# Performance work log

Hardware: AMD Instinct MI355X
Metric: run time of the kernel (lower is better)

## Reference

```python
import jax, jax.numpy as jnp
import numpy as np
from math import factorial, sqrt

L_MAX = 3
MUL = 64
# e3nn FullyConnectedTensorProduct instruction order: lexicographic over (l1, l2, l3)
# keeping paths with triangle inequality and matching parity ((-1)^(l1+l2) == (-1)^l3).
PATHS = [(l1, l2, l3)
         for l1 in range(L_MAX + 1)
         for l2 in range(L_MAX + 1)
         for l3 in range(L_MAX + 1)
         if abs(l1 - l2) <= l3 <= l1 + l2 and (l1 + l2 + l3) % 2 == 0]
assert len(PATHS) == 23
N_TO = {l3: sum(1 for p in PATHS if p[2] == l3) for l3 in range(L_MAX + 1)}


def _su2_cg(j1, m1, j2, m2, j3, m3):
    # Complex-basis Clebsch-Gordan coefficient (Racah formula), as in e3nn.
    if m3 != m1 + m2:
        return 0.0
    f = factorial
    vmin = max(-j1 + j2 + m3, -j1 + m1, 0)
    vmax = min(j2 + j3 + m1, j3 - j1 + j2, j3 + m3)
    c = sqrt((2 * j3 + 1) * f(j3 + j1 - j2) * f(j3 - j1 + j2) * f(j1 + j2 - j3)
             * f(j3 + m3) * f(j3 - m3)
             / (f(j1 + j2 + j3 + 1) * f(j1 - m1) * f(j1 + m1) * f(j2 - m2) * f(j2 + m2)))
    s = 0.0
    for v in range(vmin, vmax + 1):
        s += (-1) ** (v + j2 + m2) / f(v) * f(j2 + j3 + m1 - v) * f(j1 - m1 + v) \
             / f(j3 - j1 + j2 - v) / f(j3 + m3 - v) / f(v + j1 - j2 - m3)
    return c * s


def _q(l):
    # Change of basis real -> complex spherical harmonics (e3nn convention).
    q = np.zeros((2 * l + 1, 2 * l + 1), dtype=np.complex128)
    for m in range(-l, 0):
        q[l + m, l + abs(m)] = 1.0 / np.sqrt(2.0)
        q[l + m, l - abs(m)] = -1j / np.sqrt(2.0)
    q[l, l] = 1.0
    for m in range(1, l + 1):
        q[l + m, l + abs(m)] = (-1) ** m / np.sqrt(2.0)
        q[l + m, l - abs(m)] = 1j * (-1) ** m / np.sqrt(2.0)
    return (-1j) ** l * q


def _w3j(l1, l2, l3):
    # Real-basis Wigner 3j tensor, unit Frobenius norm (e3nn's o3.wigner_3j).
    csu2 = np.zeros((2 * l1 + 1, 2 * l2 + 1, 2 * l3 + 1))
    for m1 in range(-l1, l1 + 1):
        for m2 in range(-l2, l2 + 1):
            m3 = m1 + m2
            if -l3 <= m3 <= l3:
                csu2[l1 + m1, l2 + m2, l3 + m3] = _su2_cg(l1, m1, l2, m2, l3, m3)
    q1, q2, q3 = _q(l1), _q(l2), _q(l3)
    c = np.einsum('ij,kl,mn,ikn->jlm', q1, q2, np.conj(q3.T), csu2.astype(np.complex128))
    c = np.real(c)
    return (c / np.linalg.norm(c)).astype(np.float32)


W3J = {p: jnp.asarray(_w3j(*p)) for p in PATHS}
# e3nn 'component' irrep_normalization + 'element' path_normalization:
# per-path coeff = sqrt(ir_out.dim / (n_paths_into_out * mul1 * mul2)).
COEFF = {p: float(np.sqrt((2 * p[2] + 1) / (N_TO[p[2]] * MUL * MUL))) for p in PATHS}


def setup_inputs():
    key = jax.random.key(0)
    kx, kw = jax.random.split(key)
    x = jax.random.normal(kx, (2, 1024, MUL * (L_MAX + 1) ** 2), dtype=jnp.float32)
    weights = jax.random.normal(kw, (len(PATHS), MUL, MUL, MUL), dtype=jnp.float32)
    return {"x": x, "weights": weights}


def reference(x, weights):
    B, N, D = x.shape
    Z = B * N
    xf = x.reshape(Z, D)
    # e3nn layout: blocks of (mul, 2l+1) concatenated over l; offset = MUL * l^2.
    xs = [xf[:, MUL * l * l: MUL * (l + 1) ** 2].reshape(Z, MUL, 2 * l + 1)
          for l in range(L_MAX + 1)]
    acc = [jnp.zeros((Z, MUL, 2 * l + 1), dtype=x.dtype) for l in range(L_MAX + 1)]
    for p, (l1, l2, l3) in enumerate(PATHS):
        c = W3J[(l1, l2, l3)]
        t1 = jnp.einsum('zui,ijk->zujk', xs[l1], c)            # [Z,u,2l2+1,2l3+1]
        t2 = jnp.einsum('zujk,zvj->zuvk', t1, xs[l2])          # [Z,u,v,2l3+1]
        seg = jnp.einsum('zuvk,uvw->zwk', t2, weights[p]) * COEFF[(l1, l2, l3)]
        acc[l3] = acc[l3] + seg
    out = jnp.concatenate([a.reshape(Z, -1) for a in acc], axis=-1)
    return out.reshape(B, N, -1)
```

## Files before the change

kernel.cpp:

```cpp
#include <hip/hip_runtime.h>

struct CD { double re, im; };
constexpr CD cmul(CD a, CD b){ return CD{a.re*b.re - a.im*b.im, a.re*b.im + a.im*b.re}; }
constexpr CD conj_(CD a){ return CD{a.re, -a.im}; }

constexpr double factd(int n){ double r = 1.0; for(int i = 2; i <= n; ++i) r *= (double)i; return r; }
constexpr double csqrt_(double x){
  if (x <= 0.0) return 0.0;
  double g = x > 1.0 ? x : 1.0;
  for (int i = 0; i < 100; ++i) g = 0.5*(g + x/g);
  return g;
}

constexpr double su2_cg(int j1,int m1,int j2,int m2,int j3,int m3){
  if (m3 != m1 + m2) return 0.0;
  int vmin = -j1 + j2 + m3;
  if (-j1 + m1 > vmin) vmin = -j1 + m1;
  if (0 > vmin) vmin = 0;
  int vmax = j2 + j3 + m1;
  if (j3 - j1 + j2 < vmax) vmax = j3 - j1 + j2;
  if (j3 + m3 < vmax) vmax = j3 + m3;
  double c = csqrt_((2.0*j3 + 1.0) * factd(j3 + j1 - j2) * factd(j3 - j1 + j2) * factd(j1 + j2 - j3)
                    * factd(j3 + m3) * factd(j3 - m3)
                    / (factd(j1 + j2 + j3 + 1) * factd(j1 - m1) * factd(j1 + m1)
                       * factd(j2 - m2) * factd(j2 + m2)));
  double s = 0.0;
  for (int v = vmin; v <= vmax; ++v){
    double t = (((v + j2 + m2) & 1) ? -1.0 : 1.0) / factd(v)
               * factd(j2 + j3 + m1 - v) * factd(j1 - m1 + v)
               / factd(j3 - j1 + j2 - v) / factd(j3 + m3 - v) / factd(v + j1 - j2 - m3);
    s += t;
  }
  return c * s;
}

struct QM { CD m[7][7]; };
constexpr QM qmat(int l){
  QM q{};
  double is2 = 1.0 / csqrt_(2.0);
  for (int mm = -l; mm < 0; ++mm){
    q.m[l+mm][l-mm] = CD{is2, 0.0};
    q.m[l+mm][l+mm] = CD{0.0, -is2};
  }
  q.m[l][l] = CD{1.0, 0.0};
  for (int mm = 1; mm <= l; ++mm){
    double sgn = (mm & 1) ? -1.0 : 1.0;
    q.m[l+mm][l+mm] = CD{sgn*is2, 0.0};
    q.m[l+mm][l-mm] = CD{0.0, sgn*is2};
  }
  CD ph = (l % 4 == 0) ? CD{1,0} : (l % 4 == 1) ? CD{0,-1} : (l % 4 == 2) ? CD{-1,0} : CD{0,1};
  for (int r = 0; r < 7; ++r)
    for (int c = 0; c < 7; ++c)
      q.m[r][c] = cmul(ph, q.m[r][c]);
  return q;
}

template<int L1,int L2,int L3> struct W3JT { float v[2*L1+1][2*L2+1][2*L3+1]; };

template<int L1,int L2,int L3>
constexpr W3JT<L1,L2,L3> make_w3j(){
  constexpr int D1 = 2*L1+1, D2 = 2*L2+1, D3 = 2*L3+1;
  QM q1 = qmat(L1), q2 = qmat(L2), q3 = qmat(L3);
  double cg[7][7] = {};
  for (int i = 0; i < D1; ++i)
    for (int k = 0; k < D2; ++k){
      int n = i + k - L1 - L2 + L3;
      if (n >= 0 && n < D3) cg[i][k] = su2_cg(L1, i-L1, L2, k-L2, L3, (i-L1)+(k-L2));
    }
  double c[D1][D2][D3] = {};
  double norm2 = 0.0;
  for (int j = 0; j < D1; ++j)
    for (int l = 0; l < D2; ++l)
      for (int m = 0; m < D3; ++m){
        CD s{0.0, 0.0};
        for (int i = 0; i < D1; ++i)
          for (int k = 0; k < D2; ++k){
            double g = cg[i][k];
            if (g == 0.0) continue;
            int n = i + k - L1 - L2 + L3;
            CD t = cmul(q1.m[i][j], q2.m[k][l]);
            t = cmul(t, conj_(q3.m[n][m]));
            s.re += t.re * g; s.im += t.im * g;
          }
        c[j][l][m] = s.re;
        norm2 += s.re * s.re;
      }
  double inv = 1.0 / csqrt_(norm2);
  W3JT<L1,L2,L3> w{};
  for (int j = 0; j < D1; ++j)
    for (int l = 0; l < D2; ++l)
      for (int m = 0; m < D3; ++m){
        double val = c[j][l][m] * inv;
        if (val < 1e-10 && val > -1e-10) val = 0.0;
        w.v[j][l][m] = (float)val;
      }
  return w;
}

__device__ __constant__ int L3P_[23]  = {0,1,2,3,1,0,2,1,3,2,2,1,3,0,2,1,3,3,2,1,3,0,2};
__device__ __constant__ int SWAPP_[23] = {0,1,1,1,0,0,0,1,1,1,0,0,0,0,0,1,1,0,0,0,0,0,0};
constexpr int K3CUM[24] = {0,1,4,9,16,19,20,25,28,35,40,45,48,55,56,61,64,71,78,83,86,93,94,99};
constexpr size_t KSLICE = 2048ull * 64ull;

typedef __bf16 bf16x8 __attribute__((ext_vector_type(8)));
typedef float  f32x4  __attribute__((ext_vector_type(4)));
typedef float  f32x2  __attribute__((ext_vector_type(2)));

__global__ void pack_w_kernel(const float* __restrict__ w, unsigned short* __restrict__ wp, int total){
  int idx = blockIdx.x * 256 + threadIdx.x;
  if (idx >= total) return;
  int e    = idx & 7;
  int lane = (idx >> 3) & 63;
  int nt   = (idx >> 9) & 3;
  int hf   = (idx >> 11) & 1;
  int s    = (idx >> 12) & 63;
  int p    = idx >> 18;
  int kv = hf*32 + (lane >> 4)*8 + e;
  int wc = nt*16 + (lane & 15);
  int l3 = L3P_[p];
  const float nto[4] = {4.f, 6.f, 7.f, 6.f};
  float coeff = sqrtf((2.f*l3 + 1.f) / (nto[l3] * 4096.f));
  int a = SWAPP_[p] ? kv : s;
  int b = SWAPP_[p] ? s : kv;
  float val = w[(((size_t)p*64 + a)*64 + b)*64 + wc] * coeff;
  unsigned bits = __builtin_bit_cast(unsigned, val);
  unsigned r = (bits + 0x7FFFu + ((bits >> 16) & 1u)) >> 16;
  wp[idx] = (unsigned short)r;
}

__global__ void transpose_x(const float* __restrict__ x, float* __restrict__ xT){
  __shared__ float t[32][33];
  int bx = blockIdx.x, by = blockIdx.y;
  int tx = threadIdx.x & 31, ty = threadIdx.x >> 5;
  #pragma unroll
  for (int r = 0; r < 4; ++r)
    t[ty + r*8][tx] = x[(size_t)(by*32 + ty + r*8)*1024 + bx*32 + tx];
  __syncthreads();
  #pragma unroll
  for (int r = 0; r < 4; ++r)
    xT[(size_t)(bx*32 + ty + r*8)*2048 + by*32 + tx] = t[tx][ty + r*8];
}

template<int P,int L1,int L2,int L3,bool SWAP,int G0,int G,bool PART>
__device__ __forceinline__ void run_slot(
    int tile, const float* __restrict__ xT,
    const unsigned short* __restrict__ wp,
    float* __restrict__ dst, float* red)
{
  constexpr int K3 = 2*L3+1;
  constexpr int LK = SWAP ? L1 : L2;
  constexpr int LS = SWAP ? L2 : L1;
  constexpr int DK = 2*LK+1, DS = 2*LS+1;
  constexpr auto C = make_w3j<L1,L2,L3>();

  const int lane = threadIdx.x & 63;
  const int wv   = threadIdx.x >> 6;
  const int zc   = tile*16 + (lane & 15);

  f32x2 xk2[4][DK];
  {
    const float* xkb = xT + (size_t)(64*LK*LK)*2048 + zc;
    const int t0 = wv*32 + (lane >> 4)*8;
    #pragma unroll
    for (int q = 0; q < 4; ++q)
      #pragma unroll
      for (int t = 0; t < DK; ++t){
        float lo = xkb[(size_t)((t0 + 2*q    )*DK + t)*2048];
        float hi = xkb[(size_t)((t0 + 2*q + 1)*DK + t)*2048];
        xk2[q][t] = f32x2{lo, hi};
      }
  }

  const float* xsb = xT + (size_t)(64*LS*LS)*2048 + zc;
  const unsigned short* wu = wp + (size_t)P*262144 + (size_t)wv*2048 + (size_t)lane*8;

  f32x4 acc[G][4];
  #pragma unroll
  for (int a = 0; a < G; ++a)
    #pragma unroll
    for (int b = 0; b < 4; ++b) acc[a][b] = f32x4{0.f,0.f,0.f,0.f};

  auto compute = [&](const bf16x8 (&bf)[4], const float (&xs)[DS]){
    #pragma unroll
    for (int kk = 0; kk < G; ++kk){
      float dk[DK];
      #pragma unroll
      for (int t = 0; t < DK; ++t) dk[t] = 0.f;
      #pragma unroll
      for (int t = 0; t < DK; ++t){
        #pragma unroll
        for (int j = 0; j < DS; ++j){
          const float cv = SWAP ? C.v[t][j][G0+kk] : C.v[j][t][G0+kk];
          if (cv != 0.0f) dk[t] = __builtin_fmaf(xs[j], cv, dk[t]);
        }
      }
      f32x2 af2[4];
      #pragma unroll
      for (int q = 0; q < 4; ++q) af2[q] = f32x2{0.f, 0.f};
      #pragma unroll
      for (int t = 0; t < DK; ++t){
        const f32x2 d2 = f32x2{dk[t], dk[t]};
        #pragma unroll
        for (int q = 0; q < 4; ++q)
          af2[q] += xk2[q][t] * d2;
      }
      bf16x8 af;
      #pragma unroll
      for (int q = 0; q < 4; ++q){
        af[2*q]   = (__bf16)af2[q].x;
        af[2*q+1] = (__bf16)af2[q].y;
      }
      __builtin_amdgcn_s_setprio(1);
      #pragma unroll
      for (int nt = 0; nt < 4; ++nt)
        acc[kk][nt] = __builtin_amdgcn_mfma_f32_16x16x32_bf16(af, bf[nt], acc[kk][nt], 0, 0, 0);
      __builtin_amdgcn_s_setprio(0);
    }
  };

  bf16x8 bA[4], bB[4];
  float xsA[DS], xsB[DS];
  #pragma unroll
  for (int nt = 0; nt < 4; ++nt)
    bA[nt] = *reinterpret_cast<const bf16x8*>(wu + nt*512);
  #pragma unroll
  for (int j = 0; j < DS; ++j) xsA[j] = xsb[(size_t)j*2048];

  for (int s = 0; s < 64; s += 2){
    #pragma unroll
    for (int nt = 0; nt < 4; ++nt)
      bB[nt] = *reinterpret_cast<const bf16x8*>(wu + 4096 + nt*512);
    #pragma unroll
    for (int j = 0; j < DS; ++j) xsB[j] = xsb[(size_t)(DS + j)*2048];

    compute(bA, xsA);

    #pragma unroll
    for (int nt = 0; nt < 4; ++nt)
      bA[nt] = *reinterpret_cast<const bf16x8*>(wu + 8192 + nt*512);
    #pragma unroll
    for (int j = 0; j < DS; ++j) xsA[j] = xsb[(size_t)(2*DS + j)*2048];

    compute(bB, xsB);

    wu  += 8192;
    xsb += (size_t)2*DS*2048;
  }

  constexpr int Gh = (G + 1) / 2;
  static_assert(Gh <= 3, "red[] sized for Gh<=3");
  auto store_one = [&](int kk, int nt, const f32x4& o, const f32x4& a){
    #pragma unroll
    for (int r = 0; r < 4; ++r){
      int zl = ((lane >> 4) << 2) + r;
      int wc = nt*16 + (lane & 15);
      float val = a[r] + o[r];
      if constexpr (PART){
        dst[(size_t)(K3CUM[P] + G0 + kk)*KSLICE + (size_t)(tile*16 + zl)*64 + wc] = val;
      } else {
        unsafeAtomicAdd(dst + (size_t)(tile*16 + zl)*1024 + 64*L3*L3 + wc*K3 + (G0+kk), val);
      }
    }
  };

  if (wv == 1){
    #pragma unroll
    for (int kk = 0; kk < Gh; ++kk)
      #pragma unroll
      for (int nt = 0; nt < 4; ++nt)
        *reinterpret_cast<f32x4*>(&red[((kk*4 + nt)*64 + lane)*4]) = acc[kk][nt];
  }
  __syncthreads();
  if (wv == 0){
    #pragma unroll
    for (int kk = 0; kk < Gh; ++kk)
      #pragma unroll
      for (int nt = 0; nt < 4; ++nt){
        f32x4 o = *reinterpret_cast<const f32x4*>(&red[((kk*4 + nt)*64 + lane)*4]);
        store_one(kk, nt, o, acc[kk][nt]);
      }
  }
  if constexpr (G > Gh){
    if (wv == 0){
      #pragma unroll
      for (int kk = Gh; kk < G; ++kk)
        #pragma unroll
        for (int nt = 0; nt < 4; ++nt)
          *reinterpret_cast<f32x4*>(&red[(((kk-Gh)*4 + nt)*64 + lane)*4]) = acc[kk][nt];
    }
    __syncthreads();
    if (wv == 1){
      #pragma unroll
      for (int kk = Gh; kk < G; ++kk)
        #pragma unroll
        for (int nt = 0; nt < 4; ++nt){
          f32x4 o = *reinterpret_cast<const f32x4*>(&red[(((kk-Gh)*4 + nt)*64 + lane)*4]);
          store_one(kk, nt, o, acc[kk][nt]);
        }
    }
  }
}

template<bool PART>
__global__ __launch_bounds__(128, 3) void tp_main(const float* __restrict__ xT,
    const unsigned short* __restrict__ wp, float* __restrict__ dst)
{
  __shared__ __align__(16) float red[3072];
  const int slot = blockIdx.x >> 7;
  const int tile = blockIdx.x & 127;
  switch (slot){
    case 0:  run_slot< 6,1,1,2,false,0,5,PART>(tile,xT,wp,dst,red); break;
    case 1:  run_slot<16,2,3,3,true ,0,3,PART>(tile,xT,wp,dst,red); break;
    case 2:  run_slot<20,3,2,3,false,0,3,PART>(tile,xT,wp,dst,red); break;
    case 3:  run_slot<14,2,2,2,false,0,3,PART>(tile,xT,wp,dst,red); break;
    case 4:  run_slot<15,2,3,1,true ,0,3,PART>(tile,xT,wp,dst,red); break;
    case 5:  run_slot<19,3,2,1,false,0,3,PART>(tile,xT,wp,dst,red); break;
    case 6:  run_slot< 8,1,2,3,true ,0,4,PART>(tile,xT,wp,dst,red); break;
    case 7:  run_slot<12,2,1,3,false,0,4,PART>(tile,xT,wp,dst,red); break;
    case 8:  run_slot<22,3,3,2,false,0,2,PART>(tile,xT,wp,dst,red); break;
    case 9:  run_slot<22,3,3,2,false,2,2,PART>(tile,xT,wp,dst,red); break;
    case 10: run_slot< 9,1,3,2,true ,0,3,PART>(tile,xT,wp,dst,red); break;
    case 11: run_slot<16,2,3,3,true ,3,2,PART>(tile,xT,wp,dst,red); break;
    case 12: run_slot<16,2,3,3,true ,5,2,PART>(tile,xT,wp,dst,red); break;
    case 13: run_slot<20,3,2,3,false,3,2,PART>(tile,xT,wp,dst,red); break;
    case 14: run_slot<20,3,2,3,false,5,2,PART>(tile,xT,wp,dst,red); break;
    case 15: run_slot< 2,0,2,2,true ,0,5,PART>(tile,xT,wp,dst,red); break;
    case 16: run_slot<10,2,0,2,false,0,5,PART>(tile,xT,wp,dst,red); break;
    case 17: run_slot<11,2,1,1,false,0,3,PART>(tile,xT,wp,dst,red); break;
    case 18: run_slot< 7,1,2,1,true ,0,3,PART>(tile,xT,wp,dst,red); break;
    case 19: run_slot<18,3,1,2,false,0,3,PART>(tile,xT,wp,dst,red); break;
    case 20: run_slot< 8,1,2,3,true ,4,3,PART>(tile,xT,wp,dst,red); break;
    case 21: run_slot<12,2,1,3,false,4,3,PART>(tile,xT,wp,dst,red); break;
    case 22: run_slot<14,2,2,2,false,3,2,PART>(tile,xT,wp,dst,red); break;
    case 23: run_slot< 9,1,3,2,true ,3,2,PART>(tile,xT,wp,dst,red); break;
    case 24: run_slot<18,3,1,2,false,3,2,PART>(tile,xT,wp,dst,red); break;
    case 25: run_slot<22,3,3,2,false,4,1,PART>(tile,xT,wp,dst,red); break;
    case 26: run_slot<21,3,3,0,false,0,1,PART>(tile,xT,wp,dst,red); break;
    case 27: run_slot< 3,0,3,3,true ,0,4,PART>(tile,xT,wp,dst,red); break;
    case 28: run_slot<17,3,0,3,false,0,4,PART>(tile,xT,wp,dst,red); break;
    case 29: run_slot< 3,0,3,3,true ,4,3,PART>(tile,xT,wp,dst,red); break;
    case 30: run_slot<17,3,0,3,false,4,3,PART>(tile,xT,wp,dst,red); break;
    case 31: run_slot< 1,0,1,1,true ,0,3,PART>(tile,xT,wp,dst,red); break;
    case 32: run_slot< 4,1,0,1,false,0,3,PART>(tile,xT,wp,dst,red); break;
    case 33: run_slot<13,2,2,0,false,0,1,PART>(tile,xT,wp,dst,red); break;
    case 34: run_slot< 5,1,1,0,false,0,1,PART>(tile,xT,wp,dst,red); break;
    case 35: run_slot< 0,0,0,0,false,0,1,PART>(tile,xT,wp,dst,red); break;
    default: break;
  }
}

__global__ void gather_out(const float* __restrict__ part, float* __restrict__ out){
  const int z = blockIdx.x;
  const int t = threadIdx.x;
  const int w = t & 63;
  const int g = t >> 6;
  const size_t zw = (size_t)z*64 + w;
  const float* pb = part;
  auto rd = [&](int kg){ return pb[(size_t)kg*KSLICE + zw]; };
  float* ob = out + (size_t)z*1024;
  if (g == 0){
    ob[w] = rd(K3CUM[0]) + rd(K3CUM[5]) + rd(K3CUM[13]) + rd(K3CUM[21]);
  } else if (g == 1){
    #pragma unroll
    for (int k = 0; k < 3; ++k)
      ob[64 + w*3 + k] = rd(K3CUM[1]+k) + rd(K3CUM[4]+k) + rd(K3CUM[7]+k)
                       + rd(K3CUM[11]+k) + rd(K3CUM[15]+k) + rd(K3CUM[19]+k);
  } else if (g == 2){
    #pragma unroll
    for (int k = 0; k < 5; ++k)
      ob[256 + w*5 + k] = rd(K3CUM[2]+k) + rd(K3CUM[6]+k) + rd(K3CUM[9]+k)
                        + rd(K3CUM[10]+k) + rd(K3CUM[14]+k) + rd(K3CUM[18]+k)
                        + rd(K3CUM[22]+k);
  } else {
    #pragma unroll
    for (int k = 0; k < 7; ++k)
      ob[576 + w*7 + k] = rd(K3CUM[3]+k) + rd(K3CUM[8]+k) + rd(K3CUM[12]+k)
                        + rd(K3CUM[16]+k) + rd(K3CUM[17]+k) + rd(K3CUM[20]+k);
  }
}

extern "C" void kernel_launch(void* const* d_in, const int* in_sizes, int n_in,
                              void* d_out, int out_size, void* d_ws, size_t ws_size,
                              hipStream_t stream)
{
  const float* x = (const float*)d_in[0];
  const float* w = (const float*)d_in[1];
  float* out = (float*)d_out;

  const size_t packB = 23ull*64*2*4*64*8 * sizeof(unsigned short);
  const size_t xTB   = 1024ull*2048*sizeof(float);
  const size_t partB = 99ull*KSLICE*sizeof(float);
  const size_t slack = 65536;
  const int totalW = 23*64*2*4*64*8;

  unsigned short* wp = (unsigned short*)d_ws;
  float* xT   = (float*)((char*)d_ws + packB);
  float* part = (float*)((char*)d_ws + packB + xTB);

  if (ws_size < packB + xTB + slack) return;

  pack_w_kernel<<<(totalW + 255)/256, 256, 0, stream>>>(w, wp, totalW);
  dim3 tg(32, 64);
  transpose_x<<<tg, 256, 0, stream>>>(x, xT);

  if (ws_size >= packB + xTB + partB + slack){
    tp_main<true><<<36*128, 128, 0, stream>>>(xT, wp, part);
    gather_out<<<2048, 256, 0, stream>>>(part, out);
  } else {
    hipMemsetAsync(d_out, 0, (size_t)out_size * sizeof(float), stream);
    tp_main<false><<<36*128, 128, 0, stream>>>(xT, wp, out);
  }
}
```

Measured before the change: 222.7 us.

## Restage partial outputs through LDS for coalesced stores, simplify k-loop prefetch

Partial-sum writes are now staged per wave through a padded LDS tile, so each row of 64 output columns goes to global memory as one coalesced store. The partial buffer layout becomes z-major with the k3 index interleaved, and gather_out reads it with k-contiguous addressing. The main loop drops the manual two-stage ping-pong and becomes a single-step loop that prefetches only the next x slice. Weight fragments are now loaded in the same iteration that uses them, which may expose load latency, and the larger LDS footprint may reduce occupancy.

```diff
diff --git a/kernel.cpp b/kernel.cpp
--- a/kernel.cpp
+++ b/kernel.cpp
@@ -100,7 +100,7 @@
 __device__ __constant__ int L3P_[23]  = {0,1,2,3,1,0,2,1,3,2,2,1,3,0,2,1,3,3,2,1,3,0,2};
 __device__ __constant__ int SWAPP_[23] = {0,1,1,1,0,0,0,1,1,1,0,0,0,0,0,1,1,0,0,0,0,0,0};
 constexpr int K3CUM[24] = {0,1,4,9,16,19,20,25,28,35,40,45,48,55,56,61,64,71,78,83,86,93,94,99};
-constexpr size_t KSLICE = 2048ull * 64ull;
+constexpr size_t PSLICE = 2048ull * 64ull;
 
 typedef __bf16 bf16x8 __attribute__((ext_vector_type(8)));
 typedef float  f32x4  __attribute__((ext_vector_type(4)));
@@ -145,7 +145,7 @@
 __device__ __forceinline__ void run_slot(
     int tile, const float* __restrict__ xT,
     const unsigned short* __restrict__ wp,
-    float* __restrict__ dst, float* red)
+    float* __restrict__ dst, float* lds)
 {
   constexpr int K3 = 2*L3+1;
   constexpr int LK = SWAP ? L1 : L2;
@@ -156,6 +156,8 @@
   const int lane = threadIdx.x & 63;
   const int wv   = threadIdx.x >> 6;
   const int zc   = tile*16 + (lane & 15);
+  float* red = lds;
+  float* tl  = lds + 3072 + wv*1040;
 
   f32x2 xk2[4][DK];
   {
@@ -171,7 +173,7 @@
       }
   }
 
-  const float* xsb = xT + (size_t)(64*LS*LS)*2048 + zc;
+  const float* xsp = xT + (size_t)(64*LS*LS)*2048 + zc;
   const unsigned short* wu = wp + (size_t)P*262144 + (size_t)wv*2048 + (size_t)lane*8;
 
   f32x4 acc[G][4];
@@ -180,7 +182,21 @@
     #pragma unroll
     for (int b = 0; b < 4; ++b) acc[a][b] = f32x4{0.f,0.f,0.f,0.f};
 
-  auto compute = [&](const bf16x8 (&bf)[4], const float (&xs)[DS]){
+  float xs[DS];
+  #pragma unroll
+  for (int j = 0; j < DS; ++j) xs[j] = xsp[(size_t)j*2048];
+
+  for (int s = 0; s < 64; ++s){
+    bf16x8 bfrag[4];
+    #pragma unroll
+    for (int nt = 0; nt < 4; ++nt)
+      bfrag[nt] = *reinterpret_cast<const bf16x8*>(wu + nt*512);
+
+    const float* xnp = (s < 63) ? xsp + (size_t)DS*2048 : xsp;
+    float xn[DS];
+    #pragma unroll
+    for (int j = 0; j < DS; ++j) xn[j] = xnp[(size_t)j*2048];
+
     #pragma unroll
     for (int kk = 0; kk < G; ++kk){
       float dk[DK];
@@ -213,53 +229,39 @@
       __builtin_amdgcn_s_setprio(1);
       #pragma unroll
       for (int nt = 0; nt < 4; ++nt)
-        acc[kk][nt] = __builtin_amdgcn_mfma_f32_16x16x32_bf16(af, bf[nt], acc[kk][nt], 0, 0, 0);
+        acc[kk][nt] = __builtin_amdgcn_mfma_f32_16x16x32_bf16(af, bfrag[nt], acc[kk][nt], 0, 0, 0);
       __builtin_amdgcn_s_setprio(0);
     }
-  };
-
-  bf16x8 bA[4], bB[4];
-  float xsA[DS], xsB[DS];
-  #pragma unroll
-  for (int nt = 0; nt < 4; ++nt)
-    bA[nt] = *reinterpret_cast<const bf16x8*>(wu + nt*512);
-  #pragma unroll
-  for (int j = 0; j < DS; ++j) xsA[j] = xsb[(size_t)j*2048];
-
-  for (int s = 0; s < 64; s += 2){
-    #pragma unroll
-    for (int nt = 0; nt < 4; ++nt)
-      bB[nt] = *reinterpret_cast<const bf16x8*>(wu + 4096 + nt*512);
-    #pragma unroll
-    for (int j = 0; j < DS; ++j) xsB[j] = xsb[(size_t)(DS + j)*2048];
-
-    compute(bA, xsA);
-
-    #pragma unroll
-    for (int nt = 0; nt < 4; ++nt)
-      bA[nt] = *reinterpret_cast<const bf16x8*>(wu + 8192 + nt*512);
-    #pragma unroll
-    for (int j = 0; j < DS; ++j) xsA[j] = xsb[(size_t)(2*DS + j)*2048];
-
-    compute(bB, xsB);
-
-    wu  += 8192;
-    xsb += (size_t)2*DS*2048;
+    #pragma unroll
+    for (int j = 0; j < DS; ++j) xs[j] = xn[j];
+    xsp += (size_t)DS*2048;
+    wu  += 4096;
   }
 
   constexpr int Gh = (G + 1) / 2;
   static_assert(Gh <= 3, "red[] sized for Gh<=3");
-  auto store_one = [&](int kk, int nt, const f32x4& o, const f32x4& a){
-    #pragma unroll
-    for (int r = 0; r < 4; ++r){
-      int zl = ((lane >> 4) << 2) + r;
-      int wc = nt*16 + (lane & 15);
-      float val = a[r] + o[r];
-      if constexpr (PART){
-        dst[(size_t)(K3CUM[P] + G0 + kk)*KSLICE + (size_t)(tile*16 + zl)*64 + wc] = val;
-      } else {
-        unsafeAtomicAdd(dst + (size_t)(tile*16 + zl)*1024 + 64*L3*L3 + wc*K3 + (G0+kk), val);
-      }
+  auto store_kk = [&](int kk, const f32x4 (&sum)[4]){
+    if constexpr (PART){
+      #pragma unroll
+      for (int nt = 0; nt < 4; ++nt)
+        #pragma unroll
+        for (int r = 0; r < 4; ++r)
+          tl[(((lane >> 4)*4 + r))*65 + nt*16 + (lane & 15)] = sum[nt][r];
+      #pragma unroll
+      for (int zr = 0; zr < 16; ++zr){
+        float v = tl[zr*65 + lane];
+        dst[(size_t)K3CUM[P]*PSLICE + ((size_t)(tile*16 + zr)*K3 + (G0+kk))*64 + lane] = v;
+      }
+    } else {
+      #pragma unroll
+      for (int nt = 0; nt < 4; ++nt)
+        #pragma unroll
+        for (int r = 0; r < 4; ++r){
+          int zl = ((lane >> 4) << 2) + r;
+          int wc = nt*16 + (lane & 15);
+          unsafeAtomicAdd(dst + (size_t)(tile*16 + zl)*1024 + 64*L3*L3 + wc*K3 + (G0+kk),
+                          sum[nt][r]);
+        }
     }
   };
 
@@ -273,12 +275,15 @@
   __syncthreads();
   if (wv == 0){
     #pragma unroll
-    for (int kk = 0; kk < Gh; ++kk)
+    for (int kk = 0; kk < Gh; ++kk){
+      f32x4 sum[4];
       #pragma unroll
       for (int nt = 0; nt < 4; ++nt){
         f32x4 o = *reinterpret_cast<const f32x4*>(&red[((kk*4 + nt)*64 + lane)*4]);
-        store_one(kk, nt, o, acc[kk][nt]);
-      }
+        sum[nt] = acc[kk][nt] + o;
+      }
+      store_kk(kk, sum);
+    }
   }
   if constexpr (G > Gh){
     if (wv == 0){
@@ -291,12 +296,15 @@
     __syncthreads();
     if (wv == 1){
       #pragma unroll
-      for (int kk = Gh; kk < G; ++kk)
+      for (int kk = Gh; kk < G; ++kk){
+        f32x4 sum[4];
         #pragma unroll
         for (int nt = 0; nt < 4; ++nt){
           f32x4 o = *reinterpret_cast<const f32x4*>(&red[(((kk-Gh)*4 + nt)*64 + lane)*4]);
-          store_one(kk, nt, o, acc[kk][nt]);
+          sum[nt] = acc[kk][nt] + o;
         }
+        store_kk(kk, sum);
+      }
     }
   }
 }
@@ -305,46 +313,46 @@
 __global__ __launch_bounds__(128, 3) void tp_main(const float* __restrict__ xT,
     const unsigned short* __restrict__ wp, float* __restrict__ dst)
 {
-  __shared__ __align__(16) float red[3072];
+  __shared__ __align__(16) float lds[5152];
   const int slot = blockIdx.x >> 7;
   const int tile = blockIdx.x & 127;
   switch (slot){
-    case 0:  run_slot< 6,1,1,2,false,0,5,PART>(tile,xT,wp,dst,red); break;
-    case 1:  run_slot<16,2,3,3,true ,0,3,PART>(tile,xT,wp,dst,red); break;
-    case 2:  run_slot<20,3,2,3,false,0,3,PART>(tile,xT,wp,dst,red); break;
-    case 3:  run_slot<14,2,2,2,false,0,3,PART>(tile,xT,wp,dst,red); break;
-    case 4:  run_slot<15,2,3,1,true ,0,3,PART>(tile,xT,wp,dst,red); break;
-    case 5:  run_slot<19,3,2,1,false,0,3,PART>(tile,xT,wp,dst,red); break;
-    case 6:  run_slot< 8,1,2,3,true ,0,4,PART>(tile,xT,wp,dst,red); break;
-    case 7:  run_slot<12,2,1,3,false,0,4,PART>(tile,xT,wp,dst,red); break;
-    case 8:  run_slot<22,3,3,2,false,0,2,PART>(tile,xT,wp,dst,red); break;
-    case 9:  run_slot<22,3,3,2,false,2,2,PART>(tile,xT,wp,dst,red); break;
-    case 10: run_slot< 9,1,3,2,true ,0,3,PART>(tile,xT,wp,dst,red); break;
-    case 11: run_slot<16,2,3,3,true ,3,2,PART>(tile,xT,wp,dst,red); break;
-    case 12: run_slot<16,2,3,3,true ,5,2,PART>(tile,xT,wp,dst,red); break;
-    case 13: run_slot<20,3,2,3,false,3,2,PART>(tile,xT,wp,dst,red); break;
-    case 14: run_slot<20,3,2,3,false,5,2,PART>(tile,xT,wp,dst,red); break;
-    case 15: run_slot< 2,0,2,2,true ,0,5,PART>(tile,xT,wp,dst,red); break;
-    case 16: run_slot<10,2,0,2,false,0,5,PART>(tile,xT,wp,dst,red); break;
-    case 17: run_slot<11,2,1,1,false,0,3,PART>(tile,xT,wp,dst,red); break;
-    case 18: run_slot< 7,1,2,1,true ,0,3,PART>(tile,xT,wp,dst,red); break;
-    case 19: run_slot<18,3,1,2,false,0,3,PART>(tile,xT,wp,dst,red); break;
-    case 20: run_slot< 8,1,2,3,true ,4,3,PART>(tile,xT,wp,dst,red); break;
-    case 21: run_slot<12,2,1,3,false,4,3,PART>(tile,xT,wp,dst,red); break;
-    case 22: run_slot<14,2,2,2,false,3,2,PART>(tile,xT,wp,dst,red); break;
-    case 23: run_slot< 9,1,3,2,true ,3,2,PART>(tile,xT,wp,dst,red); break;
-    case 24: run_slot<18,3,1,2,false,3,2,PART>(tile,xT,wp,dst,red); break;
-    case 25: run_slot<22,3,3,2,false,4,1,PART>(tile,xT,wp,dst,red); break;
-    case 26: run_slot<21,3,3,0,false,0,1,PART>(tile,xT,wp,dst,red); break;
-    case 27: run_slot< 3,0,3,3,true ,0,4,PART>(tile,xT,wp,dst,red); break;
-    case 28: run_slot<17,3,0,3,false,0,4,PART>(tile,xT,wp,dst,red); break;
-    case 29: run_slot< 3,0,3,3,true ,4,3,PART>(tile,xT,wp,dst,red); break;
-    case 30: run_slot<17,3,0,3,false,4,3,PART>(tile,xT,wp,dst,red); break;
-    case 31: run_slot< 1,0,1,1,true ,0,3,PART>(tile,xT,wp,dst,red); break;
-    case 32: run_slot< 4,1,0,1,false,0,3,PART>(tile,xT,wp,dst,red); break;
-    case 33: run_slot<13,2,2,0,false,0,1,PART>(tile,xT,wp,dst,red); break;
-    case 34: run_slot< 5,1,1,0,false,0,1,PART>(tile,xT,wp,dst,red); break;
-    case 35: run_slot< 0,0,0,0,false,0,1,PART>(tile,xT,wp,dst,red); break;
+    case 0:  run_slot< 6,1,1,2,false,0,5,PART>(tile,xT,wp,dst,lds); break;
+    case 1:  run_slot<16,2,3,3,true ,0,3,PART>(tile,xT,wp,dst,lds); break;
+    case 2:  run_slot<20,3,2,3,false,0,3,PART>(tile,xT,wp,dst,lds); break;
+    case 3:  run_slot<14,2,2,2,false,0,3,PART>(tile,xT,wp,dst,lds); break;
+    case 4:  run_slot<15,2,3,1,true ,0,3,PART>(tile,xT,wp,dst,lds); break;
+    case 5:  run_slot<19,3,2,1,false,0,3,PART>(tile,xT,wp,dst,lds); break;
+    case 6:  run_slot< 8,1,2,3,true ,0,4,PART>(tile,xT,wp,dst,lds); break;
+    case 7:  run_slot<12,2,1,3,false,0,4,PART>(tile,xT,wp,dst,lds); break;
+    case 8:  run_slot<22,3,3,2,false,0,2,PART>(tile,xT,wp,dst,lds); break;
+    case 9:  run_slot<22,3,3,2,false,2,2,PART>(tile,xT,wp,dst,lds); break;
+    case 10: run_slot< 9,1,3,2,true ,0,3,PART>(tile,xT,wp,dst,lds); break;
+    case 11: run_slot<16,2,3,3,true ,3,2,PART>(tile,xT,wp,dst,lds); break;
+    case 12: run_slot<16,2,3,3,true ,5,2,PART>(tile,xT,wp,dst,lds); break;
+    case 13: run_slot<20,3,2,3,false,3,2,PART>(tile,xT,wp,dst,lds); break;
+    case 14: run_slot<20,3,2,3,false,5,2,PART>(tile,xT,wp,dst,lds); break;
+    case 15: run_slot< 2,0,2,2,true ,0,5,PART>(tile,xT,wp,dst,lds); break;
+    case 16: run_slot<10,2,0,2,false,0,5,PART>(tile,xT,wp,dst,lds); break;
+    case 17: run_slot<11,2,1,1,false,0,3,PART>(tile,xT,wp,dst,lds); break;
+    case 18: run_slot< 7,1,2,1,true ,0,3,PART>(tile,xT,wp,dst,lds); break;
+    case 19: run_slot<18,3,1,2,false,0,3,PART>(tile,xT,wp,dst,lds); break;
+    case 20: run_slot< 8,1,2,3,true ,4,3,PART>(tile,xT,wp,dst,lds); break;
+    case 21: run_slot<12,2,1,3,false,4,3,PART>(tile,xT,wp,dst,lds); break;
+    case 22: run_slot<14,2,2,2,false,3,2,PART>(tile,xT,wp,dst,lds); break;
+    case 23: run_slot< 9,1,3,2,true ,3,2,PART>(tile,xT,wp,dst,lds); break;
+    case 24: run_slot<18,3,1,2,false,3,2,PART>(tile,xT,wp,dst,lds); break;
+    case 25: run_slot<22,3,3,2,false,4,1,PART>(tile,xT,wp,dst,lds); break;
+    case 26: run_slot<21,3,3,0,false,0,1,PART>(tile,xT,wp,dst,lds); break;
+    case 27: run_slot< 3,0,3,3,true ,0,4,PART>(tile,xT,wp,dst,lds); break;
+    case 28: run_slot<17,3,0,3,false,0,4,PART>(tile,xT,wp,dst,lds); break;
+    case 29: run_slot< 3,0,3,3,true ,4,3,PART>(tile,xT,wp,dst,lds); break;
+    case 30: run_slot<17,3,0,3,false,4,3,PART>(tile,xT,wp,dst,lds); break;
+    case 31: run_slot< 1,0,1,1,true ,0,3,PART>(tile,xT,wp,dst,lds); break;
+    case 32: run_slot< 4,1,0,1,false,0,3,PART>(tile,xT,wp,dst,lds); break;
+    case 33: run_slot<13,2,2,0,false,0,1,PART>(tile,xT,wp,dst,lds); break;
+    case 34: run_slot< 5,1,1,0,false,0,1,PART>(tile,xT,wp,dst,lds); break;
+    case 35: run_slot< 0,0,0,0,false,0,1,PART>(tile,xT,wp,dst,lds); break;
     default: break;
   }
 }
@@ -354,28 +362,27 @@
   const int t = threadIdx.x;
   const int w = t & 63;
   const int g = t >> 6;
-  const size_t zw = (size_t)z*64 + w;
-  const float* pb = part;
-  auto rd = [&](int kg){ return pb[(size_t)kg*KSLICE + zw]; };
   float* ob = out + (size_t)z*1024;
+  auto rd = [&](int p, int K3p, int k){
+    return part[(size_t)K3CUM[p]*PSLICE + ((size_t)z*K3p + k)*64 + w];
+  };
   if (g == 0){
-    ob[w] = rd(K3CUM[0]) + rd(K3CUM[5]) + rd(K3CUM[13]) + rd(K3CUM[21]);
+    ob[w] = rd(0,1,0) + rd(5,1,0) + rd(13,1,0) + rd(21,1,0);
   } else if (g == 1){
     #pragma unroll
     for (int k = 0; k < 3; ++k)
-      ob[64 + w*3 + k] = rd(K3CUM[1]+k) + rd(K3CUM[4]+k) + rd(K3CUM[7]+k)
-                       + rd(K3CUM[11]+k) + rd(K3CUM[15]+k) + rd(K3CUM[19]+k);
+      ob[64 + w*3 + k] = rd(1,3,k) + rd(4,3,k) + rd(7,3,k)
+                       + rd(11,3,k) + rd(15,3,k) + rd(19,3,k);
   } else if (g == 2){
     #pragma unroll
     for (int k = 0; k < 5; ++k)
-      ob[256 + w*5 + k] = rd(K3CUM[2]+k) + rd(K3CUM[6]+k) + rd(K3CUM[9]+k)
-                        + rd(K3CUM[10]+k) + rd(K3CUM[14]+k) + rd(K3CUM[18]+k)
-                        + rd(K3CUM[22]+k);
+      ob[256 + w*5 + k] = rd(2,5,k) + rd(6,5,k) + rd(9,5,k) + rd(10,5,k)
+                        + rd(14,5,k) + rd(18,5,k) + rd(22,5,k);
   } else {
     #pragma unroll
     for (int k = 0; k < 7; ++k)
-      ob[576 + w*7 + k] = rd(K3CUM[3]+k) + rd(K3CUM[8]+k) + rd(K3CUM[12]+k)
-                        + rd(K3CUM[16]+k) + rd(K3CUM[17]+k) + rd(K3CUM[20]+k);
+      ob[576 + w*7 + k] = rd(3,7,k) + rd(8,7,k) + rd(12,7,k)
+                        + rd(16,7,k) + rd(17,7,k) + rd(20,7,k);
   }
 }
 
@@ -389,21 +396,20 @@
 
   const size_t packB = 23ull*64*2*4*64*8 * sizeof(unsigned short);
   const size_t xTB   = 1024ull*2048*sizeof(float);
-  const size_t partB = 99ull*KSLICE*sizeof(float);
-  const size_t slack = 65536;
+  const size_t partB = 99ull*PSLICE*sizeof(float);
   const int totalW = 23*64*2*4*64*8;
 
   unsigned short* wp = (unsigned short*)d_ws;
   float* xT   = (float*)((char*)d_ws + packB);
   float* part = (float*)((char*)d_ws + packB + xTB);
 
-  if (ws_size < packB + xTB + slack) return;
+  if (ws_size < packB + xTB) return;
 
   pack_w_kernel<<<(totalW + 255)/256, 256, 0, stream>>>(w, wp, totalW);
   dim3 tg(32, 64);
   transpose_x<<<tg, 256, 0, stream>>>(x, xT);
 
-  if (ws_size >= packB + xTB + partB + slack){
+  if (ws_size >= packB + xTB + partB){
     tp_main<true><<<36*128, 128, 0, stream>>>(xT, wp, part);
     gather_out<<<2048, 256, 0, stream>>>(part, out);
   } else {
```

Result: faster. 199.1 us, median of 2 (-10.6%).
